# Performance work log

Hardware: AMD Instinct MI355X
Metric: run time of the kernel (lower is better)

## Reference

```python
import jax, jax.numpy as jnp
import numpy as np

N = 100000   # nodes
E = 600000   # edges
DIN = 128
H = 128
DOUT = 64
EPS = 1e-5   # BatchNorm1d default eps


def setup_inputs() -> dict:
    key = jax.random.key(0)
    ks = jax.random.split(key, 16)
    w = lambda k, shape: jax.random.normal(k, shape, jnp.float32) * 0.05
    return {
        "x": jax.random.normal(ks[0], (N, DIN), jnp.float32),
        "edge_index": jax.random.randint(ks[1], (2, E), 0, N),
        # layer 1: SAGEConv(DIN -> H)  (lin_l on aggregated neighbors w/ bias, lin_r on root)
        "Wl1": w(ks[2], (DIN, H)), "bl1": jnp.zeros((H,), jnp.float32), "Wr1": w(ks[3], (DIN, H)),
        "g1": jnp.ones((H,), jnp.float32), "be1": jnp.zeros((H,), jnp.float32),
        "rm1": jax.random.normal(ks[4], (H,), jnp.float32) * 0.1,
        "rv1": jax.random.uniform(ks[5], (H,), jnp.float32, 0.5, 1.5),
        # layer 2: SAGEConv(H -> H)
        "Wl2": w(ks[6], (H, H)), "bl2": jnp.zeros((H,), jnp.float32), "Wr2": w(ks[7], (H, H)),
        "g2": jnp.ones((H,), jnp.float32), "be2": jnp.zeros((H,), jnp.float32),
        "rm2": jax.random.normal(ks[8], (H,), jnp.float32) * 0.1,
        "rv2": jax.random.uniform(ks[9], (H,), jnp.float32, 0.5, 1.5),
        # layer 3: SAGEConv(H -> DOUT), no BN/ReLU after
        "Wl3": w(ks[10], (H, DOUT)), "bl3": jnp.zeros((DOUT,), jnp.float32), "Wr3": w(ks[11], (H, DOUT)),
    }


def _sage_conv(x, src, dst, Wl, bl, Wr):
    # mean-aggregate source features at targets, then lin_l(agg) + b + lin_r(x)
    agg = jax.ops.segment_sum(x[src], dst, num_segments=N)          # [N, d]
    deg = jax.ops.segment_sum(jnp.ones((src.shape[0],), x.dtype), dst, num_segments=N)
    agg = agg / jnp.maximum(deg, 1.0)[:, None]
    return agg @ Wl + bl + x @ Wr


def _bn_eval(h, g, b, rm, rv):
    return (h - rm) * (g * jax.lax.rsqrt(rv + EPS)) + b


def reference(x, edge_index, Wl1, bl1, Wr1, g1, be1, rm1, rv1,
              Wl2, bl2, Wr2, g2, be2, rm2, rv2, Wl3, bl3, Wr3):
    src, dst = edge_index[0], edge_index[1]
    h = jax.nn.relu(_bn_eval(_sage_conv(x, src, dst, Wl1, bl1, Wr1), g1, be1, rm1, rv1))
    h = jax.nn.relu(_bn_eval(_sage_conv(h, src, dst, Wl2, bl2, Wr2), g2, be2, rm2, rv2))
    return _sage_conv(h, src, dst, Wl3, bl3, Wr3)   # [N, DOUT]
```

## Files before the change

kernel.cpp:

```cpp
#include <hip/hip_runtime.h>

#define CAP 48

typedef short  s8v  __attribute__((ext_vector_type(8)));
typedef float  f4v  __attribute__((ext_vector_type(4)));

__device__ __forceinline__ unsigned short f2bf(float f) {
    unsigned u = __float_as_uint(f);
    u += 0x7FFFu + ((u >> 16) & 1u);
    return (unsigned short)(u >> 16);
}
__device__ __forceinline__ float bflo(unsigned v) { return __uint_as_float(v << 16); }
__device__ __forceinline__ float bfhi(unsigned v) { return __uint_as_float(v & 0xffff0000u); }

#define ACC8(v)  do { a[0]+=bflo((v).x); a[1]+=bfhi((v).x); a[2]+=bflo((v).y); a[3]+=bfhi((v).y); \
                      a[4]+=bflo((v).z); a[5]+=bfhi((v).z); a[6]+=bflo((v).w); a[7]+=bfhi((v).w); } while(0)

__global__ __launch_bounds__(256) void k_bucket(const int* __restrict__ src, const int* __restrict__ dst,
                                                int E, int* __restrict__ cnt, int* __restrict__ bucket) {
    int e = blockIdx.x * 256 + threadIdx.x;
    if (e < E) {
        int d = dst[e];
        int slot = atomicAdd(&cnt[d], 1);
        if (slot < CAP) bucket[(size_t)d * CAP + slot] = src[e];
    }
}

__global__ __launch_bounds__(256) void k_prepack(const float* W0, const float* W1, const float* W2,
                                                 const float* W3, const float* W4, const float* W5,
                                                 unsigned short* P0, unsigned short* P1, unsigned short* P2,
                                                 unsigned short* P3, unsigned short* P4, unsigned short* P5,
                                                 const float* g1, const float* be1, const float* rm1, const float* rv1, const float* bl1,
                                                 const float* g2, const float* be2, const float* rm2, const float* rv2, const float* bl2,
                                                 float* P,
                                                 unsigned short* xb, unsigned short* hb, unsigned short* hb2,
                                                 unsigned short* t3b, int N) {
    if (blockIdx.y == 6) {
        if (blockIdx.x == 0) {
            int i = threadIdx.x;
            if (i < 128) {
                float s1 = g1[i] * rsqrtf(rv1[i] + 1e-5f);
                P[i]       = s1;
                P[128 + i] = (bl1[i] - rm1[i]) * s1 + be1[i];
                float s2 = g2[i] * rsqrtf(rv2[i] + 1e-5f);
                P[256 + i] = s2;
                P[384 + i] = (bl2[i] - rm2[i]) * s2 + be2[i];
                xb [(size_t)N * 128 + i] = 0;
                hb [(size_t)N * 128 + i] = 0;
                hb2[(size_t)N * 128 + i] = 0;
                if (i < 64) t3b[(size_t)N * 64 + i] = 0;
            }
        }
        return;
    }
    const float* W; unsigned short* Pk; int JD;
    switch (blockIdx.y) {
        case 0: W = W0; Pk = P0; JD = 128; break;
        case 1: W = W1; Pk = P1; JD = 128; break;
        case 2: W = W2; Pk = P2; JD = 128; break;
        case 3: W = W3; Pk = P3; JD = 128; break;
        case 4: W = W4; Pk = P4; JD = 64;  break;
        default:W = W5; Pk = P5; JD = 64;  break;
    }
    int o = blockIdx.x * 256 + threadIdx.x;
    if (o >= 128 * JD) return;
    int j    = o & 7;
    int lane = (o >> 3) & 63;
    int t    = o >> 9;
    int nt   = t % (JD / 16);
    int kt   = t / (JD / 16);
    int k = kt * 32 + (lane >> 4) * 8 + j;
    int n = nt * 16 + (lane & 15);
    Pk[o] = f2bf(W[(size_t)k * JD + n]);
}

__global__ __launch_bounds__(256) void k_cvt(const float* __restrict__ in, unsigned short* __restrict__ out, int n4) {
    int i = blockIdx.x * 256 + threadIdx.x;
    if (i < n4) {
        float4 v = ((const float4*)in)[i];
        ushort4 o;
        o.x = f2bf(v.x); o.y = f2bf(v.y); o.z = f2bf(v.z); o.w = f2bf(v.w);
        ((ushort4*)out)[i] = o;
    }
}

template<bool T3>
__global__ __launch_bounds__(256) void k_fused(const unsigned short* __restrict__ feat,
                                               const int* __restrict__ cnt, const int* __restrict__ bucket,
                                               const unsigned short* __restrict__ Bl, const unsigned short* __restrict__ Br,
                                               const float* __restrict__ scale, const float* __restrict__ shift,
                                               unsigned short* __restrict__ out,
                                               const unsigned short* __restrict__ W3p, unsigned short* __restrict__ t3,
                                               int n) {
    __shared__ unsigned short sA[32 * 136];
    __shared__ unsigned short sH[T3 ? 32 * 136 : 8];
    const int tid  = threadIdx.x;
    const int wave = tid >> 6;
    const int lane = tid & 63;
    const int nb0  = blockIdx.x * 32;
    if (nb0 >= n) return;

    {
        const int q4   = lane >> 4;
        const int li   = lane & 15;
        const int base = q4 << 4;
        const uint4* inp = (const uint4*)feat;
        int rows[2], cs[2], idxs[2];
        #pragma unroll
        for (int t = 0; t < 2; t++) {
            rows[t] = wave * 8 + t * 4 + q4;
            int node = nb0 + rows[t];
            bool ok = node < n;
            int c = ok ? cnt[node] : 0; if (c > CAP) c = CAP;
            cs[t] = c;
            idxs[t] = (ok && li < c) ? bucket[(size_t)node * CAP + li] : n;
        }
        #pragma unroll
        for (int t = 0; t < 2; t++) {
            const int c = cs[t];
            float a[8] = {0.f, 0.f, 0.f, 0.f, 0.f, 0.f, 0.f, 0.f};
            if (c > 0) {
                #pragma unroll
                for (int u = 0; u < 8; u++) {
                    int idx = __shfl(idxs[t], base + u);
                    uint4 v = inp[(size_t)idx * 16 + li];
                    ACC8(v);
                }
            }
            if (c > 8) {
                #pragma unroll
                for (int u = 8; u < 16; u++) {
                    int idx = __shfl(idxs[t], base + u);
                    uint4 v = inp[(size_t)idx * 16 + li];
                    ACC8(v);
                }
            }
            const int node = nb0 + rows[t];
            for (int s = 16; s < c; s++) {
                int idx = bucket[(size_t)node * CAP + s];
                uint4 v = inp[(size_t)idx * 16 + li];
                ACC8(v);
            }
            if (node < n) {
                float iv = 1.0f / fmaxf((float)c, 1.0f);
                uint4 o;
                o.x = (unsigned)f2bf(a[0] * iv) | ((unsigned)f2bf(a[1] * iv) << 16);
                o.y = (unsigned)f2bf(a[2] * iv) | ((unsigned)f2bf(a[3] * iv) << 16);
                o.z = (unsigned)f2bf(a[4] * iv) | ((unsigned)f2bf(a[5] * iv) << 16);
                o.w = (unsigned)f2bf(a[6] * iv) | ((unsigned)f2bf(a[7] * iv) << 16);
                *(uint4*)(sA + rows[t] * 136 + li * 8) = o;
            }
        }
    }
    __syncthreads();

    const int m = lane & 15;
    const int q = lane >> 4;
    const int nt0 = wave * 2;
    const int rg0 = min(nb0 + m,      n - 1);
    const int rg1 = min(nb0 + 16 + m, n - 1);

    f4v acc[2][2];
    #pragma unroll
    for (int mt = 0; mt < 2; mt++)
        #pragma unroll
        for (int c = 0; c < 2; c++) {
            acc[mt][c][0] = 0.f; acc[mt][c][1] = 0.f; acc[mt][c][2] = 0.f; acc[mt][c][3] = 0.f;
        }

    #pragma unroll
    for (int kt = 0; kt < 4; kt++) {
        const int ko = kt * 32 + q * 8;
        s8v a0 = *(const s8v*)(sA + m * 136 + ko);
        s8v a1 = *(const s8v*)(sA + (16 + m) * 136 + ko);
        s8v a0d = *(const s8v*)(feat + (size_t)rg0 * 128 + ko);
        s8v a1d = *(const s8v*)(feat + (size_t)rg1 * 128 + ko);
        #pragma unroll
        for (int c = 0; c < 2; c++) {
            s8v b  = *(const s8v*)(Bl + ((size_t)(kt * 8 + nt0 + c) * 64 + lane) * 8);
            acc[0][c] = __builtin_amdgcn_mfma_f32_16x16x32_bf16(a0, b, acc[0][c], 0, 0, 0);
            acc[1][c] = __builtin_amdgcn_mfma_f32_16x16x32_bf16(a1, b, acc[1][c], 0, 0, 0);
            s8v b2 = *(const s8v*)(Br + ((size_t)(kt * 8 + nt0 + c) * 64 + lane) * 8);
            acc[0][c] = __builtin_amdgcn_mfma_f32_16x16x32_bf16(a0d, b2, acc[0][c], 0, 0, 0);
            acc[1][c] = __builtin_amdgcn_mfma_f32_16x16x32_bf16(a1d, b2, acc[1][c], 0, 0, 0);
        }
    }

    float scv[2], shv[2];
    #pragma unroll
    for (int c = 0; c < 2; c++) {
        int col = (nt0 + c) * 16 + m;
        scv[c] = scale[col]; shv[c] = shift[col];
    }
    #pragma unroll
    for (int mt = 0; mt < 2; mt++) {
        #pragma unroll
        for (int reg = 0; reg < 4; reg++) {
            int rloc = mt * 16 + q * 4 + reg;
            int row  = nb0 + rloc;
            if (row < n) {
                #pragma unroll
                for (int c = 0; c < 2; c++) {
                    int col = (nt0 + c) * 16 + m;
                    float v = fmaxf(acc[mt][c][reg] * scv[c] + shv[c], 0.f);
                    unsigned short u = f2bf(v);
                    out[(size_t)row * 128 + col] = u;
                    if constexpr (T3) sH[rloc * 136 + col] = u;
                }
            }
        }
    }

    if constexpr (T3) {
        __syncthreads();
        f4v a3c[2];
        #pragma unroll
        for (int mt = 0; mt < 2; mt++) { a3c[mt][0] = 0.f; a3c[mt][1] = 0.f; a3c[mt][2] = 0.f; a3c[mt][3] = 0.f; }
        #pragma unroll
        for (int kt = 0; kt < 4; kt++) {
            const int ko = kt * 32 + q * 8;
            s8v a0 = *(const s8v*)(sH + m * 136 + ko);
            s8v a1 = *(const s8v*)(sH + (16 + m) * 136 + ko);
            s8v b  = *(const s8v*)(W3p + ((size_t)(kt * 4 + wave) * 64 + lane) * 8);
            a3c[0] = __builtin_amdgcn_mfma_f32_16x16x32_bf16(a0, b, a3c[0], 0, 0, 0);
            a3c[1] = __builtin_amdgcn_mfma_f32_16x16x32_bf16(a1, b, a3c[1], 0, 0, 0);
        }
        #pragma unroll
        for (int mt = 0; mt < 2; mt++) {
            #pragma unroll
            for (int reg = 0; reg < 4; reg++) {
                int row = nb0 + mt * 16 + q * 4 + reg;
                if (row < n) t3[(size_t)row * 64 + wave * 16 + m] = f2bf(a3c[mt][reg]);
            }
        }
    }
}

__global__ __launch_bounds__(256) void k_final(const unsigned short* __restrict__ hb2,
                                               const unsigned short* __restrict__ t3,
                                               const int* __restrict__ cnt, const int* __restrict__ bucket,
                                               const unsigned short* __restrict__ Bp, const float* __restrict__ bias,
                                               float* __restrict__ outf, int n) {
    __shared__ float sG[32 * 68];
    const int tid  = threadIdx.x;
    const int wave = tid >> 6;
    const int lane = tid & 63;
    const int nb0  = blockIdx.x * 32;
    if (nb0 >= n) return;

    {
        const int e8   = lane >> 3;
        const int li   = lane & 7;
        const int base = e8 << 3;
        const uint4* inp = (const uint4*)t3;
        const int row  = wave * 8 + e8;
        const int node = nb0 + row;
        const bool ok  = node < n;
        int c = ok ? cnt[node] : 0; if (c > CAP) c = CAP;
        int idx1 = (ok && li < c)     ? bucket[(size_t)node * CAP + li]     : n;
        int idx2 = (ok && li + 8 < c) ? bucket[(size_t)node * CAP + li + 8] : n;
        float a[8] = {0.f, 0.f, 0.f, 0.f, 0.f, 0.f, 0.f, 0.f};
        if (c > 0) {
            #pragma unroll
            for (int u = 0; u < 8; u++) {
                int idx = __shfl(idx1, base + u);
                uint4 v = inp[(size_t)idx * 8 + li];
                ACC8(v);
            }
        }
        if (c > 8) {
            #pragma unroll
            for (int u = 0; u < 8; u++) {
                int idx = __shfl(idx2, base + u);
                uint4 v = inp[(size_t)idx * 8 + li];
                ACC8(v);
            }
        }
        for (int s = 16; s < c; s++) {
            int idx = bucket[(size_t)node * CAP + s];
            uint4 v = inp[(size_t)idx * 8 + li];
            ACC8(v);
        }
        if (ok) {
            float iv = 1.0f / fmaxf((float)c, 1.0f);
            float4 o1; o1.x = a[0] * iv; o1.y = a[1] * iv; o1.z = a[2] * iv; o1.w = a[3] * iv;
            float4 o2; o2.x = a[4] * iv; o2.y = a[5] * iv; o2.z = a[6] * iv; o2.w = a[7] * iv;
            *(float4*)(sG + row * 68 + li * 8)     = o1;
            *(float4*)(sG + row * 68 + li * 8 + 4) = o2;
        }
    }
    __syncthreads();

    const int m = lane & 15;
    const int q = lane >> 4;
    const int rg0 = min(nb0 + m,      n - 1);
    const int rg1 = min(nb0 + 16 + m, n - 1);

    f4v acc[2];
    #pragma unroll
    for (int mt = 0; mt < 2; mt++) { acc[mt][0] = 0.f; acc[mt][1] = 0.f; acc[mt][2] = 0.f; acc[mt][3] = 0.f; }

    #pragma unroll
    for (int kt = 0; kt < 4; kt++) {
        const int ko = kt * 32 + q * 8;
        s8v a0 = *(const s8v*)(hb2 + (size_t)rg0 * 128 + ko);
        s8v a1 = *(const s8v*)(hb2 + (size_t)rg1 * 128 + ko);
        s8v b  = *(const s8v*)(Bp + ((size_t)(kt * 4 + wave) * 64 + lane) * 8);
        acc[0] = __builtin_amdgcn_mfma_f32_16x16x32_bf16(a0, b, acc[0], 0, 0, 0);
        acc[1] = __builtin_amdgcn_mfma_f32_16x16x32_bf16(a1, b, acc[1], 0, 0, 0);
    }

    const int col = wave * 16 + m;
    const float bv = bias[col];
    #pragma unroll
    for (int mt = 0; mt < 2; mt++) {
        #pragma unroll
        for (int reg = 0; reg < 4; reg++) {
            int rloc = mt * 16 + q * 4 + reg;
            int row  = nb0 + rloc;
            if (row < n) outf[(size_t)row * 64 + col] = acc[mt][reg] + sG[rloc * 68 + col] + bv;
        }
    }
}

extern "C" void kernel_launch(void* const* d_in, const int* in_sizes, int n_in,
                              void* d_out, int out_size, void* d_ws, size_t ws_size,
                              hipStream_t stream) {
    const float* x   = (const float*)d_in[0];
    const int*   ei  = (const int*)d_in[1];
    const float* Wl1 = (const float*)d_in[2];
    const float* bl1 = (const float*)d_in[3];
    const float* Wr1 = (const float*)d_in[4];
    const float* g1  = (const float*)d_in[5];
    const float* be1 = (const float*)d_in[6];
    const float* rm1 = (const float*)d_in[7];
    const float* rv1 = (const float*)d_in[8];
    const float* Wl2 = (const float*)d_in[9];
    const float* bl2 = (const float*)d_in[10];
    const float* Wr2 = (const float*)d_in[11];
    const float* g2  = (const float*)d_in[12];
    const float* be2 = (const float*)d_in[13];
    const float* rm2 = (const float*)d_in[14];
    const float* rv2 = (const float*)d_in[15];
    const float* Wl3 = (const float*)d_in[16];
    const float* bl3 = (const float*)d_in[17];
    const float* Wr3 = (const float*)d_in[18];

    const int N = in_sizes[0] / 128;
    const int E = in_sizes[1] / 2;
    const int* src = ei;
    const int* dst = ei + E;

    char* w = (char*)d_ws;
    auto au = [](size_t v) { return (v + 1023) & ~(size_t)1023; };
    size_t off = 0;
    int*            cnt    = (int*)(w + off);            off += au((size_t)N * 4);
    int*            bucket = (int*)(w + off);            off += au((size_t)N * CAP * 4);
    unsigned short* xb     = (unsigned short*)(w + off); off += au((size_t)(N + 1) * 128 * 2);
    unsigned short* hb     = (unsigned short*)(w + off); off += au((size_t)(N + 1) * 128 * 2);
    unsigned short* hb2    = (unsigned short*)(w + off); off += au((size_t)(N + 1) * 128 * 2);
    unsigned short* t3b    = (unsigned short*)(w + off); off += au((size_t)(N + 1) * 64 * 2);
    unsigned short* Wp[6];
    Wp[0] = (unsigned short*)(w + off); off += au(128 * 128 * 2);
    Wp[1] = (unsigned short*)(w + off); off += au(128 * 128 * 2);
    Wp[2] = (unsigned short*)(w + off); off += au(128 * 128 * 2);
    Wp[3] = (unsigned short*)(w + off); off += au(128 * 128 * 2);
    Wp[4] = (unsigned short*)(w + off); off += au(128 * 64 * 2);
    Wp[5] = (unsigned short*)(w + off); off += au(128 * 64 * 2);
    float* P = (float*)(w + off); off += 2048;
    (void)ws_size; (void)n_in;

    hipMemsetAsync(cnt, 0, (size_t)N * 4, stream);
    k_bucket<<<(E + 255) / 256, 256, 0, stream>>>(src, dst, E, cnt, bucket);
    dim3 pg(64, 7);
    k_prepack<<<pg, 256, 0, stream>>>(Wl1, Wr1, Wl2, Wr2, Wl3, Wr3,
                                      Wp[0], Wp[1], Wp[2], Wp[3], Wp[4], Wp[5],
                                      g1, be1, rm1, rv1, bl1, g2, be2, rm2, rv2, bl2, P,
                                      xb, hb, hb2, t3b, N);
    k_cvt<<<((N * 128 / 4) + 255) / 256, 256, 0, stream>>>(x, xb, N * 128 / 4);

    const int grid = (N + 31) / 32;

    k_fused<false><<<grid, 256, 0, stream>>>(xb, cnt, bucket, Wp[0], Wp[1],
                                             P, P + 128, hb, nullptr, nullptr, N);
    k_fused<true><<<grid, 256, 0, stream>>>(hb, cnt, bucket, Wp[2], Wp[3],
                                            P + 256, P + 384, hb2, Wp[4], t3b, N);
    k_final<<<grid, 256, 0, stream>>>(hb2, t3b, cnt, bucket, Wp[5], bl3, (float*)d_out, N);
}
```

Baseline: 297.0 us.

## Merge prep kernels into one launch and software-pipeline neighbor gather loads

Combines the bucketing, fp32-to-bf16 conversion and weight prepacking kernels into a single launch with block-range dispatch, removing two launch gaps. In the fused and final kernels, the neighbor gather now issues the next batch of eight row loads before accumulating the previous batch, overlapping memory latency with ALU work across both rows handled by a wave. Branching on neighbor count now uses wave-uniform __any predicates, so waves always load the first eight neighbors (padding entries point at the zero row). This raises register pressure from the eight-element uint4 buffer.

```diff
diff --git a/kernel.cpp b/kernel.cpp
--- a/kernel.cpp
+++ b/kernel.cpp
@@ -13,48 +13,64 @@
 __device__ __forceinline__ float bflo(unsigned v) { return __uint_as_float(v << 16); }
 __device__ __forceinline__ float bfhi(unsigned v) { return __uint_as_float(v & 0xffff0000u); }
 
-#define ACC8(v)  do { a[0]+=bflo((v).x); a[1]+=bfhi((v).x); a[2]+=bflo((v).y); a[3]+=bfhi((v).y); \
-                      a[4]+=bflo((v).z); a[5]+=bfhi((v).z); a[6]+=bflo((v).w); a[7]+=bfhi((v).w); } while(0)
-
-__global__ __launch_bounds__(256) void k_bucket(const int* __restrict__ src, const int* __restrict__ dst,
-                                                int E, int* __restrict__ cnt, int* __restrict__ bucket) {
-    int e = blockIdx.x * 256 + threadIdx.x;
-    if (e < E) {
-        int d = dst[e];
-        int slot = atomicAdd(&cnt[d], 1);
-        if (slot < CAP) bucket[(size_t)d * CAP + slot] = src[e];
-    }
-}
-
-__global__ __launch_bounds__(256) void k_prepack(const float* W0, const float* W1, const float* W2,
-                                                 const float* W3, const float* W4, const float* W5,
-                                                 unsigned short* P0, unsigned short* P1, unsigned short* P2,
-                                                 unsigned short* P3, unsigned short* P4, unsigned short* P5,
-                                                 const float* g1, const float* be1, const float* rm1, const float* rv1, const float* bl1,
-                                                 const float* g2, const float* be2, const float* rm2, const float* rv2, const float* bl2,
-                                                 float* P,
-                                                 unsigned short* xb, unsigned short* hb, unsigned short* hb2,
-                                                 unsigned short* t3b, int N) {
-    if (blockIdx.y == 6) {
-        if (blockIdx.x == 0) {
-            int i = threadIdx.x;
-            if (i < 128) {
-                float s1 = g1[i] * rsqrtf(rv1[i] + 1e-5f);
-                P[i]       = s1;
-                P[128 + i] = (bl1[i] - rm1[i]) * s1 + be1[i];
-                float s2 = g2[i] * rsqrtf(rv2[i] + 1e-5f);
-                P[256 + i] = s2;
-                P[384 + i] = (bl2[i] - rm2[i]) * s2 + be2[i];
-                xb [(size_t)N * 128 + i] = 0;
-                hb [(size_t)N * 128 + i] = 0;
-                hb2[(size_t)N * 128 + i] = 0;
-                if (i < 64) t3b[(size_t)N * 64 + i] = 0;
-            }
+#define ACC8(A, v) do { (A)[0]+=bflo((v).x); (A)[1]+=bfhi((v).x); (A)[2]+=bflo((v).y); (A)[3]+=bfhi((v).y); \
+                        (A)[4]+=bflo((v).z); (A)[5]+=bfhi((v).z); (A)[6]+=bflo((v).w); (A)[7]+=bfhi((v).w); } while(0)
+
+__global__ __launch_bounds__(256) void k_prep(const int* __restrict__ src, const int* __restrict__ dst, int E,
+                                              int* __restrict__ cnt, int* __restrict__ bucket,
+                                              const float* __restrict__ x, unsigned short* __restrict__ xb, int n4,
+                                              const float* W0, const float* W1, const float* W2,
+                                              const float* W3, const float* W4, const float* W5,
+                                              unsigned short* P0, unsigned short* P1, unsigned short* P2,
+                                              unsigned short* P3, unsigned short* P4, unsigned short* P5,
+                                              const float* g1, const float* be1, const float* rm1, const float* rv1, const float* bl1,
+                                              const float* g2, const float* be2, const float* rm2, const float* rv2, const float* bl2,
+                                              float* P,
+                                              unsigned short* hb, unsigned short* hb2, unsigned short* t3b, int N,
+                                              int nbBucket, int nbCvt) {
+    int b = blockIdx.x;
+    const int tid = threadIdx.x;
+    if (b < nbBucket) {
+        int e = b * 256 + tid;
+        if (e < E) {
+            int d = dst[e];
+            int slot = atomicAdd(&cnt[d], 1);
+            if (slot < CAP) bucket[(size_t)d * CAP + slot] = src[e];
         }
         return;
     }
+    b -= nbBucket;
+    if (b < nbCvt) {
+        int i = b * 256 + tid;
+        if (i < n4) {
+            float4 v = ((const float4*)x)[i];
+            ushort4 o;
+            o.x = f2bf(v.x); o.y = f2bf(v.y); o.z = f2bf(v.z); o.w = f2bf(v.w);
+            ((ushort4*)xb)[i] = o;
+        }
+        return;
+    }
+    b -= nbCvt;
+    const int px = b & 63;
+    const int py = b >> 6;
+    if (py == 6) {
+        if (px == 0 && tid < 128) {
+            int i = tid;
+            float s1 = g1[i] * rsqrtf(rv1[i] + 1e-5f);
+            P[i]       = s1;
+            P[128 + i] = (bl1[i] - rm1[i]) * s1 + be1[i];
+            float s2 = g2[i] * rsqrtf(rv2[i] + 1e-5f);
+            P[256 + i] = s2;
+            P[384 + i] = (bl2[i] - rm2[i]) * s2 + be2[i];
+            xb [(size_t)N * 128 + i] = 0;
+            hb [(size_t)N * 128 + i] = 0;
+            hb2[(size_t)N * 128 + i] = 0;
+            if (i < 64) t3b[(size_t)N * 64 + i] = 0;
+        }
+        return;
+    }
     const float* W; unsigned short* Pk; int JD;
-    switch (blockIdx.y) {
+    switch (py) {
         case 0: W = W0; Pk = P0; JD = 128; break;
         case 1: W = W1; Pk = P1; JD = 128; break;
         case 2: W = W2; Pk = P2; JD = 128; break;
@@ -62,7 +78,7 @@
         case 4: W = W4; Pk = P4; JD = 64;  break;
         default:W = W5; Pk = P5; JD = 64;  break;
     }
-    int o = blockIdx.x * 256 + threadIdx.x;
+    int o = px * 256 + tid;
     if (o >= 128 * JD) return;
     int j    = o & 7;
     int lane = (o >> 3) & 63;
@@ -70,18 +86,8 @@
     int nt   = t % (JD / 16);
     int kt   = t / (JD / 16);
     int k = kt * 32 + (lane >> 4) * 8 + j;
-    int n = nt * 16 + (lane & 15);
-    Pk[o] = f2bf(W[(size_t)k * JD + n]);
-}
-
-__global__ __launch_bounds__(256) void k_cvt(const float* __restrict__ in, unsigned short* __restrict__ out, int n4) {
-    int i = blockIdx.x * 256 + threadIdx.x;
-    if (i < n4) {
-        float4 v = ((const float4*)in)[i];
-        ushort4 o;
-        o.x = f2bf(v.x); o.y = f2bf(v.y); o.z = f2bf(v.z); o.w = f2bf(v.w);
-        ((ushort4*)out)[i] = o;
-    }
+    int nn = nt * 16 + (lane & 15);
+    Pk[o] = f2bf(W[(size_t)k * JD + nn]);
 }
 
 template<bool T3>
@@ -115,40 +121,79 @@
             cs[t] = c;
             idxs[t] = (ok && li < c) ? bucket[(size_t)node * CAP + li] : n;
         }
-        #pragma unroll
-        for (int t = 0; t < 2; t++) {
-            const int c = cs[t];
-            float a[8] = {0.f, 0.f, 0.f, 0.f, 0.f, 0.f, 0.f, 0.f};
-            if (c > 0) {
-                #pragma unroll
-                for (int u = 0; u < 8; u++) {
-                    int idx = __shfl(idxs[t], base + u);
-                    uint4 v = inp[(size_t)idx * 16 + li];
-                    ACC8(v);
-                }
-            }
-            if (c > 8) {
-                #pragma unroll
-                for (int u = 8; u < 16; u++) {
-                    int idx = __shfl(idxs[t], base + u);
-                    uint4 v = inp[(size_t)idx * 16 + li];
-                    ACC8(v);
-                }
-            }
-            const int node = nb0 + rows[t];
+        const bool anyB0 = __any(cs[0] > 8);
+        const bool anyB1 = __any(cs[1] > 8);
+
+        float a0[8] = {0.f, 0.f, 0.f, 0.f, 0.f, 0.f, 0.f, 0.f};
+        float a1[8] = {0.f, 0.f, 0.f, 0.f, 0.f, 0.f, 0.f, 0.f};
+        uint4 v[8];
+
+        #pragma unroll
+        for (int u = 0; u < 8; u++) {
+            int idx = __shfl(idxs[0], base + u);
+            v[u] = inp[(size_t)idx * 16 + li];
+        }
+        if (anyB0) {
+            #pragma unroll
+            for (int u = 0; u < 8; u++) {
+                uint4 t = v[u];
+                int idx = __shfl(idxs[0], base + 8 + u);
+                v[u] = inp[(size_t)idx * 16 + li];
+                ACC8(a0, t);
+            }
+        }
+        #pragma unroll
+        for (int u = 0; u < 8; u++) {
+            uint4 t = v[u];
+            int idx = __shfl(idxs[1], base + u);
+            v[u] = inp[(size_t)idx * 16 + li];
+            ACC8(a0, t);
+        }
+        {
+            const int c = cs[0];
+            const int node = nb0 + rows[0];
             for (int s = 16; s < c; s++) {
                 int idx = bucket[(size_t)node * CAP + s];
-                uint4 v = inp[(size_t)idx * 16 + li];
-                ACC8(v);
+                uint4 t = inp[(size_t)idx * 16 + li];
+                ACC8(a0, t);
             }
             if (node < n) {
                 float iv = 1.0f / fmaxf((float)c, 1.0f);
                 uint4 o;
-                o.x = (unsigned)f2bf(a[0] * iv) | ((unsigned)f2bf(a[1] * iv) << 16);
-                o.y = (unsigned)f2bf(a[2] * iv) | ((unsigned)f2bf(a[3] * iv) << 16);
-                o.z = (unsigned)f2bf(a[4] * iv) | ((unsigned)f2bf(a[5] * iv) << 16);
-                o.w = (unsigned)f2bf(a[6] * iv) | ((unsigned)f2bf(a[7] * iv) << 16);
-                *(uint4*)(sA + rows[t] * 136 + li * 8) = o;
+                o.x = (unsigned)f2bf(a0[0] * iv) | ((unsigned)f2bf(a0[1] * iv) << 16);
+                o.y = (unsigned)f2bf(a0[2] * iv) | ((unsigned)f2bf(a0[3] * iv) << 16);
+                o.z = (unsigned)f2bf(a0[4] * iv) | ((unsigned)f2bf(a0[5] * iv) << 16);
+                o.w = (unsigned)f2bf(a0[6] * iv) | ((unsigned)f2bf(a0[7] * iv) << 16);
+                *(uint4*)(sA + rows[0] * 136 + li * 8) = o;
+            }
+        }
+        if (anyB1) {
+            #pragma unroll
+            for (int u = 0; u < 8; u++) {
+                uint4 t = v[u];
+                int idx = __shfl(idxs[1], base + 8 + u);
+                v[u] = inp[(size_t)idx * 16 + li];
+                ACC8(a1, t);
+            }
+        }
+        #pragma unroll
+        for (int u = 0; u < 8; u++) ACC8(a1, v[u]);
+        {
+            const int c = cs[1];
+            const int node = nb0 + rows[1];
+            for (int s = 16; s < c; s++) {
+                int idx = bucket[(size_t)node * CAP + s];
+                uint4 t = inp[(size_t)idx * 16 + li];
+                ACC8(a1, t);
+            }
+            if (node < n) {
+                float iv = 1.0f / fmaxf((float)c, 1.0f);
+                uint4 o;
+                o.x = (unsigned)f2bf(a1[0] * iv) | ((unsigned)f2bf(a1[1] * iv) << 16);
+                o.y = (unsigned)f2bf(a1[2] * iv) | ((unsigned)f2bf(a1[3] * iv) << 16);
+                o.z = (unsigned)f2bf(a1[4] * iv) | ((unsigned)f2bf(a1[5] * iv) << 16);
+                o.w = (unsigned)f2bf(a1[6] * iv) | ((unsigned)f2bf(a1[7] * iv) << 16);
+                *(uint4*)(sA + rows[1] * 136 + li * 8) = o;
             }
         }
     }
@@ -259,27 +304,29 @@
         int c = ok ? cnt[node] : 0; if (c > CAP) c = CAP;
         int idx1 = (ok && li < c)     ? bucket[(size_t)node * CAP + li]     : n;
         int idx2 = (ok && li + 8 < c) ? bucket[(size_t)node * CAP + li + 8] : n;
+        const bool anyB = __any(c > 8);
         float a[8] = {0.f, 0.f, 0.f, 0.f, 0.f, 0.f, 0.f, 0.f};
-        if (c > 0) {
+        uint4 v[8];
+        #pragma unroll
+        for (int u = 0; u < 8; u++) {
+            int idx = __shfl(idx1, base + u);
+            v[u] = inp[(size_t)idx * 8 + li];
+        }
+        if (anyB) {
             #pragma unroll
             for (int u = 0; u < 8; u++) {
-                int idx = __shfl(idx1, base + u);
-                uint4 v = inp[(size_t)idx * 8 + li];
-                ACC8(v);
-            }
-        }
-        if (c > 8) {
-            #pragma unroll
-            for (int u = 0; u < 8; u++) {
+                uint4 t = v[u];
                 int idx = __shfl(idx2, base + u);
-                uint4 v = inp[(size_t)idx * 8 + li];
-                ACC8(v);
-            }
-        }
+                v[u] = inp[(size_t)idx * 8 + li];
+                ACC8(a, t);
+            }
+        }
+        #pragma unroll
+        for (int u = 0; u < 8; u++) ACC8(a, v[u]);
         for (int s = 16; s < c; s++) {
             int idx = bucket[(size_t)node * CAP + s];
-            uint4 v = inp[(size_t)idx * 8 + li];
-            ACC8(v);
+            uint4 t = inp[(size_t)idx * 8 + li];
+            ACC8(a, t);
         }
         if (ok) {
             float iv = 1.0f / fmaxf((float)c, 1.0f);
@@ -371,13 +418,16 @@
     (void)ws_size; (void)n_in;
 
     hipMemsetAsync(cnt, 0, (size_t)N * 4, stream);
-    k_bucket<<<(E + 255) / 256, 256, 0, stream>>>(src, dst, E, cnt, bucket);
-    dim3 pg(64, 7);
-    k_prepack<<<pg, 256, 0, stream>>>(Wl1, Wr1, Wl2, Wr2, Wl3, Wr3,
-                                      Wp[0], Wp[1], Wp[2], Wp[3], Wp[4], Wp[5],
-                                      g1, be1, rm1, rv1, bl1, g2, be2, rm2, rv2, bl2, P,
-                                      xb, hb, hb2, t3b, N);
-    k_cvt<<<((N * 128 / 4) + 255) / 256, 256, 0, stream>>>(x, xb, N * 128 / 4);
+
+    const int n4 = N * 128 / 4;
+    const int nbBucket = (E + 255) / 256;
+    const int nbCvt    = (n4 + 255) / 256;
+    k_prep<<<nbBucket + nbCvt + 448, 256, 0, stream>>>(src, dst, E, cnt, bucket,
+                                                       x, xb, n4,
+                                                       Wl1, Wr1, Wl2, Wr2, Wl3, Wr3,
+                                                       Wp[0], Wp[1], Wp[2], Wp[3], Wp[4], Wp[5],
+                                                       g1, be1, rm1, rv1, bl1, g2, be2, rm2, rv2, bl2, P,
+                                                       hb, hb2, t3b, N, nbBucket, nbCvt);
 
     const int grid = (N + 31) / 32;
 
```

New measurement: 293.4 us. No clear change (-1.2%).

## Merge all stages into one persistent cooperative kernel with grid syncs

Applied to the files above, without the earlier changes.

Replaces six separate launches (bucket, prepack, cvt, two fused layers, final) with one cooperative persistent kernel. Blocks loop over work units and a grid-wide barrier separates the phases, removing per-launch overhead and the gaps between kernels. In exchange, the grid is capped at occupancy, the launch bounds force up to eight blocks per CU (register pressure), and each phase pays a grid barrier. The dependency on the bucket and prepack results is still enforced by the barrier.

```diff
diff --git a/kernel.cpp b/kernel.cpp
--- a/kernel.cpp
+++ b/kernel.cpp
@@ -1,4 +1,5 @@
 #include <hip/hip_runtime.h>
+#include <hip/hip_cooperative_groups.h>
 
 #define CAP 48
 
@@ -13,56 +14,70 @@
 __device__ __forceinline__ float bflo(unsigned v) { return __uint_as_float(v << 16); }
 __device__ __forceinline__ float bfhi(unsigned v) { return __uint_as_float(v & 0xffff0000u); }
 
-#define ACC8(v)  do { a[0]+=bflo((v).x); a[1]+=bfhi((v).x); a[2]+=bflo((v).y); a[3]+=bfhi((v).y); \
-                      a[4]+=bflo((v).z); a[5]+=bfhi((v).z); a[6]+=bflo((v).w); a[7]+=bfhi((v).w); } while(0)
-
-__global__ __launch_bounds__(256) void k_bucket(const int* __restrict__ src, const int* __restrict__ dst,
-                                                int E, int* __restrict__ cnt, int* __restrict__ bucket) {
-    int e = blockIdx.x * 256 + threadIdx.x;
-    if (e < E) {
-        int d = dst[e];
-        int slot = atomicAdd(&cnt[d], 1);
-        if (slot < CAP) bucket[(size_t)d * CAP + slot] = src[e];
-    }
-}
-
-__global__ __launch_bounds__(256) void k_prepack(const float* W0, const float* W1, const float* W2,
-                                                 const float* W3, const float* W4, const float* W5,
-                                                 unsigned short* P0, unsigned short* P1, unsigned short* P2,
-                                                 unsigned short* P3, unsigned short* P4, unsigned short* P5,
-                                                 const float* g1, const float* be1, const float* rm1, const float* rv1, const float* bl1,
-                                                 const float* g2, const float* be2, const float* rm2, const float* rv2, const float* bl2,
-                                                 float* P,
-                                                 unsigned short* xb, unsigned short* hb, unsigned short* hb2,
-                                                 unsigned short* t3b, int N) {
-    if (blockIdx.y == 6) {
-        if (blockIdx.x == 0) {
-            int i = threadIdx.x;
-            if (i < 128) {
-                float s1 = g1[i] * rsqrtf(rv1[i] + 1e-5f);
-                P[i]       = s1;
-                P[128 + i] = (bl1[i] - rm1[i]) * s1 + be1[i];
-                float s2 = g2[i] * rsqrtf(rv2[i] + 1e-5f);
-                P[256 + i] = s2;
-                P[384 + i] = (bl2[i] - rm2[i]) * s2 + be2[i];
-                xb [(size_t)N * 128 + i] = 0;
-                hb [(size_t)N * 128 + i] = 0;
-                hb2[(size_t)N * 128 + i] = 0;
-                if (i < 64) t3b[(size_t)N * 64 + i] = 0;
-            }
+#define ACC8(A_, v) do { (A_)[0]+=bflo((v).x); (A_)[1]+=bfhi((v).x); (A_)[2]+=bflo((v).y); (A_)[3]+=bfhi((v).y); \
+                         (A_)[4]+=bflo((v).z); (A_)[5]+=bfhi((v).z); (A_)[6]+=bflo((v).w); (A_)[7]+=bfhi((v).w); } while(0)
+
+struct KArgs {
+    const int* src; const int* dst;
+    const float* x;
+    const float* W[6];
+    const float *g1, *be1, *rm1, *rv1, *bl1;
+    const float *g2, *be2, *rm2, *rv2, *bl2;
+    const float* bl3;
+    int* cnt; int* bucket;
+    unsigned short* xb; unsigned short* hb; unsigned short* hb2; unsigned short* t3b;
+    unsigned short* Wp[6];
+    float* P;
+    float* outf;
+    int N, E, nbBucket, nbCvt, nbL;
+};
+
+__device__ void prep_unit(int b, const KArgs& A) {
+    const int tid = threadIdx.x;
+    if (b < A.nbBucket) {
+        int e = b * 256 + tid;
+        if (e < A.E) {
+            int d = A.dst[e];
+            int slot = atomicAdd(A.cnt + d, 1);
+            if (slot < CAP) A.bucket[(size_t)d * CAP + slot] = A.src[e];
         }
         return;
     }
-    const float* W; unsigned short* Pk; int JD;
-    switch (blockIdx.y) {
-        case 0: W = W0; Pk = P0; JD = 128; break;
-        case 1: W = W1; Pk = P1; JD = 128; break;
-        case 2: W = W2; Pk = P2; JD = 128; break;
-        case 3: W = W3; Pk = P3; JD = 128; break;
-        case 4: W = W4; Pk = P4; JD = 64;  break;
-        default:W = W5; Pk = P5; JD = 64;  break;
-    }
-    int o = blockIdx.x * 256 + threadIdx.x;
+    b -= A.nbBucket;
+    if (b < A.nbCvt) {
+        int i = b * 256 + tid;
+        int n4 = A.N * 32;
+        if (i < n4) {
+            float4 v = ((const float4*)A.x)[i];
+            ushort4 o;
+            o.x = f2bf(v.x); o.y = f2bf(v.y); o.z = f2bf(v.z); o.w = f2bf(v.w);
+            ((ushort4*)A.xb)[i] = o;
+        }
+        return;
+    }
+    b -= A.nbCvt;
+    const int px = b & 63;
+    const int py = b >> 6;
+    if (py == 6) {
+        if (px == 0 && tid < 128) {
+            int i = tid;
+            float s1 = A.g1[i] * rsqrtf(A.rv1[i] + 1e-5f);
+            A.P[i]       = s1;
+            A.P[128 + i] = (A.bl1[i] - A.rm1[i]) * s1 + A.be1[i];
+            float s2 = A.g2[i] * rsqrtf(A.rv2[i] + 1e-5f);
+            A.P[256 + i] = s2;
+            A.P[384 + i] = (A.bl2[i] - A.rm2[i]) * s2 + A.be2[i];
+            A.xb [(size_t)A.N * 128 + i] = 0;
+            A.hb [(size_t)A.N * 128 + i] = 0;
+            A.hb2[(size_t)A.N * 128 + i] = 0;
+            if (i < 64) A.t3b[(size_t)A.N * 64 + i] = 0;
+        }
+        return;
+    }
+    const float* W = A.W[py];
+    unsigned short* Pk = A.Wp[py];
+    const int JD = (py >= 4) ? 64 : 128;
+    int o = px * 256 + tid;
     if (o >= 128 * JD) return;
     int j    = o & 7;
     int lane = (o >> 3) & 63;
@@ -70,35 +85,28 @@
     int nt   = t % (JD / 16);
     int kt   = t / (JD / 16);
     int k = kt * 32 + (lane >> 4) * 8 + j;
-    int n = nt * 16 + (lane & 15);
-    Pk[o] = f2bf(W[(size_t)k * JD + n]);
-}
-
-__global__ __launch_bounds__(256) void k_cvt(const float* __restrict__ in, unsigned short* __restrict__ out, int n4) {
-    int i = blockIdx.x * 256 + threadIdx.x;
-    if (i < n4) {
-        float4 v = ((const float4*)in)[i];
-        ushort4 o;
-        o.x = f2bf(v.x); o.y = f2bf(v.y); o.z = f2bf(v.z); o.w = f2bf(v.w);
-        ((ushort4*)out)[i] = o;
-    }
+    int nn = nt * 16 + (lane & 15);
+    Pk[o] = f2bf(W[(size_t)k * JD + nn]);
 }
 
 template<bool T3>
-__global__ __launch_bounds__(256) void k_fused(const unsigned short* __restrict__ feat,
-                                               const int* __restrict__ cnt, const int* __restrict__ bucket,
-                                               const unsigned short* __restrict__ Bl, const unsigned short* __restrict__ Br,
-                                               const float* __restrict__ scale, const float* __restrict__ shift,
-                                               unsigned short* __restrict__ out,
-                                               const unsigned short* __restrict__ W3p, unsigned short* __restrict__ t3,
-                                               int n) {
-    __shared__ unsigned short sA[32 * 136];
-    __shared__ unsigned short sH[T3 ? 32 * 136 : 8];
+__device__ void layer_unit(int u, const KArgs& A,
+                           const unsigned short* __restrict__ feat,
+                           const unsigned short* __restrict__ Bl,
+                           const unsigned short* __restrict__ Br,
+                           const float* __restrict__ scale,
+                           const float* __restrict__ shift,
+                           unsigned short* __restrict__ out,
+                           const unsigned short* __restrict__ W3p,
+                           unsigned short* __restrict__ t3,
+                           unsigned short* sA, unsigned short* sH) {
+    const int n = A.N;
+    const int* __restrict__ cnt    = A.cnt;
+    const int* __restrict__ bucket = A.bucket;
     const int tid  = threadIdx.x;
     const int wave = tid >> 6;
     const int lane = tid & 63;
-    const int nb0  = blockIdx.x * 32;
-    if (nb0 >= n) return;
+    const int nb0  = u * 32;
 
     {
         const int q4   = lane >> 4;
@@ -121,25 +129,25 @@
             float a[8] = {0.f, 0.f, 0.f, 0.f, 0.f, 0.f, 0.f, 0.f};
             if (c > 0) {
                 #pragma unroll
-                for (int u = 0; u < 8; u++) {
-                    int idx = __shfl(idxs[t], base + u);
+                for (int uu = 0; uu < 8; uu++) {
+                    int idx = __shfl(idxs[t], base + uu);
                     uint4 v = inp[(size_t)idx * 16 + li];
-                    ACC8(v);
+                    ACC8(a, v);
                 }
             }
             if (c > 8) {
                 #pragma unroll
-                for (int u = 8; u < 16; u++) {
-                    int idx = __shfl(idxs[t], base + u);
+                for (int uu = 8; uu < 16; uu++) {
+                    int idx = __shfl(idxs[t], base + uu);
                     uint4 v = inp[(size_t)idx * 16 + li];
-                    ACC8(v);
+                    ACC8(a, v);
                 }
             }
             const int node = nb0 + rows[t];
             for (int s = 16; s < c; s++) {
                 int idx = bucket[(size_t)node * CAP + s];
                 uint4 v = inp[(size_t)idx * 16 + li];
-                ACC8(v);
+                ACC8(a, v);
             }
             if (node < n) {
                 float iv = 1.0f / fmaxf((float)c, 1.0f);
@@ -203,9 +211,9 @@
                 for (int c = 0; c < 2; c++) {
                     int col = (nt0 + c) * 16 + m;
                     float v = fmaxf(acc[mt][c][reg] * scv[c] + shv[c], 0.f);
-                    unsigned short u = f2bf(v);
-                    out[(size_t)row * 128 + col] = u;
-                    if constexpr (T3) sH[rloc * 136 + col] = u;
+                    unsigned short uq = f2bf(v);
+                    out[(size_t)row * 128 + col] = uq;
+                    if constexpr (T3) sH[rloc * 136 + col] = uq;
                 }
             }
         }
@@ -236,23 +244,21 @@
     }
 }
 
-__global__ __launch_bounds__(256) void k_final(const unsigned short* __restrict__ hb2,
-                                               const unsigned short* __restrict__ t3,
-                                               const int* __restrict__ cnt, const int* __restrict__ bucket,
-                                               const unsigned short* __restrict__ Bp, const float* __restrict__ bias,
-                                               float* __restrict__ outf, int n) {
-    __shared__ float sG[32 * 68];
+__device__ void final_unit(int u, const KArgs& A, float* sG) {
+    const int n = A.N;
+    const unsigned short* __restrict__ hb2 = A.hb2;
+    const int* __restrict__ cnt    = A.cnt;
+    const int* __restrict__ bucket = A.bucket;
     const int tid  = threadIdx.x;
     const int wave = tid >> 6;
     const int lane = tid & 63;
-    const int nb0  = blockIdx.x * 32;
-    if (nb0 >= n) return;
+    const int nb0  = u * 32;
 
     {
         const int e8   = lane >> 3;
         const int li   = lane & 7;
         const int base = e8 << 3;
-        const uint4* inp = (const uint4*)t3;
+        const uint4* inp = (const uint4*)A.t3b;
         const int row  = wave * 8 + e8;
         const int node = nb0 + row;
         const bool ok  = node < n;
@@ -262,24 +268,24 @@
         float a[8] = {0.f, 0.f, 0.f, 0.f, 0.f, 0.f, 0.f, 0.f};
         if (c > 0) {
             #pragma unroll
-            for (int u = 0; u < 8; u++) {
-                int idx = __shfl(idx1, base + u);
+            for (int uu = 0; uu < 8; uu++) {
+                int idx = __shfl(idx1, base + uu);
                 uint4 v = inp[(size_t)idx * 8 + li];
-                ACC8(v);
+                ACC8(a, v);
             }
         }
         if (c > 8) {
             #pragma unroll
-            for (int u = 0; u < 8; u++) {
-                int idx = __shfl(idx2, base + u);
+            for (int uu = 0; uu < 8; uu++) {
+                int idx = __shfl(idx2, base + uu);
                 uint4 v = inp[(size_t)idx * 8 + li];
-                ACC8(v);
+                ACC8(a, v);
             }
         }
         for (int s = 16; s < c; s++) {
             int idx = bucket[(size_t)node * CAP + s];
             uint4 v = inp[(size_t)idx * 8 + li];
-            ACC8(v);
+            ACC8(a, v);
         }
         if (ok) {
             float iv = 1.0f / fmaxf((float)c, 1.0f);
@@ -305,21 +311,51 @@
         const int ko = kt * 32 + q * 8;
         s8v a0 = *(const s8v*)(hb2 + (size_t)rg0 * 128 + ko);
         s8v a1 = *(const s8v*)(hb2 + (size_t)rg1 * 128 + ko);
-        s8v b  = *(const s8v*)(Bp + ((size_t)(kt * 4 + wave) * 64 + lane) * 8);
+        s8v b  = *(const s8v*)(A.Wp[5] + ((size_t)(kt * 4 + wave) * 64 + lane) * 8);
         acc[0] = __builtin_amdgcn_mfma_f32_16x16x32_bf16(a0, b, acc[0], 0, 0, 0);
         acc[1] = __builtin_amdgcn_mfma_f32_16x16x32_bf16(a1, b, acc[1], 0, 0, 0);
     }
 
     const int col = wave * 16 + m;
-    const float bv = bias[col];
+    const float bv = A.bl3[col];
     #pragma unroll
     for (int mt = 0; mt < 2; mt++) {
         #pragma unroll
         for (int reg = 0; reg < 4; reg++) {
             int rloc = mt * 16 + q * 4 + reg;
             int row  = nb0 + rloc;
-            if (row < n) outf[(size_t)row * 64 + col] = acc[mt][reg] + sG[rloc * 68 + col] + bv;
-        }
+            if (row < n) A.outf[(size_t)row * 64 + col] = acc[mt][reg] + sG[rloc * 68 + col] + bv;
+        }
+    }
+}
+
+__global__ __launch_bounds__(256, 8) void k_all(KArgs A) {
+    __shared__ __align__(16) unsigned short sA[32 * 136];
+    __shared__ __align__(16) unsigned short sH[32 * 136];
+    cooperative_groups::grid_group gg = cooperative_groups::this_grid();
+
+    const int UA = A.nbBucket + A.nbCvt + 448;
+    for (int b = blockIdx.x; b < UA; b += gridDim.x)
+        prep_unit(b, A);
+    gg.sync();
+
+    for (int u = blockIdx.x; u < A.nbL; u += gridDim.x) {
+        layer_unit<false>(u, A, A.xb, A.Wp[0], A.Wp[1], A.P, A.P + 128,
+                          A.hb, nullptr, nullptr, sA, sH);
+        __syncthreads();
+    }
+    gg.sync();
+
+    for (int u = blockIdx.x; u < A.nbL; u += gridDim.x) {
+        layer_unit<true>(u, A, A.hb, A.Wp[2], A.Wp[3], A.P + 256, A.P + 384,
+                         A.hb2, A.Wp[4], A.t3b, sA, sH);
+        __syncthreads();
+    }
+    gg.sync();
+
+    for (int u = blockIdx.x; u < A.nbL; u += gridDim.x) {
+        final_unit(u, A, (float*)sA);
+        __syncthreads();
     }
 }
 
@@ -328,28 +364,9 @@
                               hipStream_t stream) {
     const float* x   = (const float*)d_in[0];
     const int*   ei  = (const int*)d_in[1];
-    const float* Wl1 = (const float*)d_in[2];
-    const float* bl1 = (const float*)d_in[3];
-    const float* Wr1 = (const float*)d_in[4];
-    const float* g1  = (const float*)d_in[5];
-    const float* be1 = (const float*)d_in[6];
-    const float* rm1 = (const float*)d_in[7];
-    const float* rv1 = (const float*)d_in[8];
-    const float* Wl2 = (const float*)d_in[9];
-    const float* bl2 = (const float*)d_in[10];
-    const float* Wr2 = (const float*)d_in[11];
-    const float* g2  = (const float*)d_in[12];
-    const float* be2 = (const float*)d_in[13];
-    const float* rm2 = (const float*)d_in[14];
-    const float* rv2 = (const float*)d_in[15];
-    const float* Wl3 = (const float*)d_in[16];
-    const float* bl3 = (const float*)d_in[17];
-    const float* Wr3 = (const float*)d_in[18];
 
     const int N = in_sizes[0] / 128;
     const int E = in_sizes[1] / 2;
-    const int* src = ei;
-    const int* dst = ei + E;
 
     char* w = (char*)d_ws;
     auto au = [](size_t v) { return (v + 1023) & ~(size_t)1023; };
@@ -370,20 +387,52 @@
     float* P = (float*)(w + off); off += 2048;
     (void)ws_size; (void)n_in;
 
+    KArgs A;
+    A.src = ei; A.dst = ei + E;
+    A.x   = x;
+    A.W[0] = (const float*)d_in[2];
+    A.bl1  = (const float*)d_in[3];
+    A.W[1] = (const float*)d_in[4];
+    A.g1   = (const float*)d_in[5];
+    A.be1  = (const float*)d_in[6];
+    A.rm1  = (const float*)d_in[7];
+    A.rv1  = (const float*)d_in[8];
+    A.W[2] = (const float*)d_in[9];
+    A.bl2  = (const float*)d_in[10];
+    A.W[3] = (const float*)d_in[11];
+    A.g2   = (const float*)d_in[12];
+    A.be2  = (const float*)d_in[13];
+    A.rm2  = (const float*)d_in[14];
+    A.rv2  = (const float*)d_in[15];
+    A.W[4] = (const float*)d_in[16];
+    A.bl3  = (const float*)d_in[17];
+    A.W[5] = (const float*)d_in[18];
+    A.cnt = cnt; A.bucket = bucket;
+    A.xb = xb; A.hb = hb; A.hb2 = hb2; A.t3b = t3b;
+    for (int i = 0; i < 6; i++) A.Wp[i] = Wp[i];
+    A.P = P;
+    A.outf = (float*)d_out;
+    A.N = N; A.E = E;
+    A.nbBucket = (E + 255) / 256;
+    A.nbCvt    = (N * 32 + 255) / 256;
+    A.nbL      = (N + 31) / 32;
+
+    static int gridBlocks = 0;
+    if (gridBlocks == 0) {
+        int dev = 0;
+        hipGetDevice(&dev);
+        hipDeviceProp_t prop;
+        hipGetDeviceProperties(&prop, dev);
+        int nb = 0;
+        hipOccupancyMaxActiveBlocksPerMultiprocessor(&nb, k_all, 256, 0);
+        if (nb < 1) nb = 1;
+        gridBlocks = nb * prop.multiProcessorCount;
+        if (gridBlocks > 4096) gridBlocks = 4096;
+        if (gridBlocks < 1) gridBlocks = 1;
+    }
+
     hipMemsetAsync(cnt, 0, (size_t)N * 4, stream);
-    k_bucket<<<(E + 255) / 256, 256, 0, stream>>>(src, dst, E, cnt, bucket);
-    dim3 pg(64, 7);
-    k_prepack<<<pg, 256, 0, stream>>>(Wl1, Wr1, Wl2, Wr2, Wl3, Wr3,
-                                      Wp[0], Wp[1], Wp[2], Wp[3], Wp[4], Wp[5],
-                                      g1, be1, rm1, rv1, bl1, g2, be2, rm2, rv2, bl2, P,
-                                      xb, hb, hb2, t3b, N);
-    k_cvt<<<((N * 128 / 4) + 255) / 256, 256, 0, stream>>>(x, xb, N * 128 / 4);
-
-    const int grid = (N + 31) / 32;
-
-    k_fused<false><<<grid, 256, 0, stream>>>(xb, cnt, bucket, Wp[0], Wp[1],
-                                             P, P + 128, hb, nullptr, nullptr, N);
-    k_fused<true><<<grid, 256, 0, stream>>>(hb, cnt, bucket, Wp[2], Wp[3],
-                                            P + 256, P + 384, hb2, Wp[4], t3b, N);
-    k_final<<<grid, 256, 0, stream>>>(hb2, t3b, cnt, bucket, Wp[5], bl3, (float*)d_out, N);
-}
+    void* params[] = { (void*)&A };
+    hipLaunchCooperativeKernel((const void*)k_all, dim3(gridBlocks), dim3(256),
+                               params, 0, stream);
+}
```

Result: slower. 881.5 us (+196.8%).
